# Kernel optimization log

Measured on AMD Instinct MI355X. Metric: run time of the kernel, lower is better.

## Reference

```python
import jax, jax.numpy as jnp
import numpy as np

N_HEAD = 16
N_STATE = 1024
D_HEAD = N_STATE // N_HEAD
B, T = 4, 2048


def setup_inputs() -> dict:
    key = jax.random.key(0)
    ks = jax.random.split(key, 9)
    x = jax.random.normal(ks[0], (B, T, N_STATE), dtype=jnp.float32)
    # causal additive mask, (T, T)
    neg = jnp.float32(-1e9)
    mask = jnp.where(jnp.tril(jnp.ones((T, T), dtype=bool)), 0.0, neg).astype(jnp.float32)
    s = 0.02  # keep activations in a sane range (module uses torch.randn init)
    Wq = jax.random.normal(ks[1], (N_STATE, N_STATE), dtype=jnp.float32) * s
    bq = jax.random.normal(ks[2], (N_STATE,), dtype=jnp.float32) * s
    Wk = jax.random.normal(ks[3], (N_STATE, N_STATE), dtype=jnp.float32) * s
    Wv = jax.random.normal(ks[4], (N_STATE, N_STATE), dtype=jnp.float32) * s
    bv = jax.random.normal(ks[5], (N_STATE,), dtype=jnp.float32) * s
    Wo = jax.random.normal(ks[6], (N_STATE, N_STATE), dtype=jnp.float32) * s
    bo = jax.random.normal(ks[7], (N_STATE,), dtype=jnp.float32) * s
    return {"x": x, "mask": mask, "Wq": Wq, "bq": bq, "Wk": Wk,
            "Wv": Wv, "bv": bv, "Wo": Wo, "bo": bo}


def reference(x, mask, Wq, bq, Wk, Wv, bv, Wo, bo):
    n, t, _ = x.shape
    scale = D_HEAD ** -0.25
    # projections: Linear stores weight as (out, in), applies x @ W.T
    q = x @ Wq.T + bq
    k = x @ Wk.T          # key has no bias
    v = x @ Wv.T + bv
    # (N, H, T, d)
    q = q.reshape(n, t, N_HEAD, D_HEAD).transpose(0, 2, 1, 3) * scale
    k = k.reshape(n, t, N_HEAD, D_HEAD).transpose(0, 2, 1, 3) * scale
    v = v.reshape(n, t, N_HEAD, D_HEAD).transpose(0, 2, 1, 3)
    qk = jnp.einsum('bhqd,bhkd->bhqk', q, k)
    qk = qk + mask[:t, :t]
    attn = jax.nn.softmax(qk, axis=-1)
    qkv = jnp.einsum('bhqk,bhkd->bhqd', attn, v)
    qkv = qkv.transpose(0, 2, 1, 3).reshape(n, t, N_STATE)
    return qkv @ Wo.T + bo
```

## Files before the change

### kernel.cpp

```cpp
#include <hip/hip_runtime.h>
#include <stdint.h>

#define DEVI __device__ __forceinline__

typedef float        f32x4   __attribute__((ext_vector_type(4)));
typedef float        f32x16  __attribute__((ext_vector_type(16)));
typedef __bf16       bf16x8  __attribute__((ext_vector_type(8)));
typedef unsigned short u16x8 __attribute__((ext_vector_type(8)));
typedef uint32_t     u32x2   __attribute__((ext_vector_type(2)));
typedef uint32_t     u32x4   __attribute__((ext_vector_type(4)));

static constexpr int TSEQ   = 2048;
static constexpr int NSTATE = 1024;
static constexpr int NHEAD  = 16;
static constexpr int DHEAD  = 64;
static constexpr int BATCH  = 4;
static constexpr int MROWS  = BATCH * TSEQ;
static constexpr float QSCALE = 0.125f * 1.44269504088896340736f;
static constexpr float DEFER_THR = 8.0f * 1.44269504088896340736f;

DEVI unsigned short f2bf(float f) {
  union { float f; uint32_t u; } v; v.f = f;
  return (unsigned short)((v.u + 0x7fffu + ((v.u >> 16) & 1u)) >> 16);
}

DEVI uint32_t cvt_pk_bf16(float lo, float hi) {
  uint32_t r;
  asm("v_cvt_pk_bf16_f32 %0, %1, %2" : "=v"(r) : "v"(lo), "v"(hi));
  return r;
}

DEVI f32x4 mfma16(u16x8 a, u16x8 b, f32x4 c) {
  return __builtin_amdgcn_mfma_f32_16x16x32_bf16(
      __builtin_bit_cast(bf16x8, a), __builtin_bit_cast(bf16x8, b), c, 0, 0, 0);
}
DEVI f32x16 mfma32(u16x8 a, u16x8 b, f32x16 c) {
  return __builtin_amdgcn_mfma_f32_32x32x16_bf16(
      __builtin_bit_cast(bf16x8, a), __builtin_bit_cast(bf16x8, b), c, 0, 0, 0);
}

DEVI void gload_lds16(const void* g, void* l) {
  __builtin_amdgcn_global_load_lds(
      (const __attribute__((address_space(1))) void*)g,
      (__attribute__((address_space(3))) void*)l, 16, 0, 0);
}

__global__ void cvt_kernel(const float* __restrict__ in,
                           unsigned short* __restrict__ out, int n4) {
  int i = blockIdx.x * blockDim.x + threadIdx.x;
  const int stride = gridDim.x * blockDim.x;
  for (; i < n4; i += stride) {
    const float4 f = ((const float4*)in)[i];
    ushort4 o;
    o.x = f2bf(f.x); o.y = f2bf(f.y); o.z = f2bf(f.z); o.w = f2bf(f.w);
    ((ushort4*)out)[i] = o;
  }
}

__global__ void cvt4_kernel(const float* __restrict__ w0, const float* __restrict__ w1,
                            const float* __restrict__ w2, const float* __restrict__ w3,
                            unsigned short* __restrict__ o0, unsigned short* __restrict__ o1,
                            unsigned short* __restrict__ o2, unsigned short* __restrict__ o3) {
  const int per = NSTATE * NSTATE / 4;
  int i = blockIdx.x * blockDim.x + threadIdx.x;
  const int stride = gridDim.x * blockDim.x;
  for (; i < 4 * per; i += stride) {
    const int wi = i / per, j = i - wi * per;
    const float* src = (wi == 0) ? w0 : (wi == 1) ? w1 : (wi == 2) ? w2 : w3;
    unsigned short* dst = (wi == 0) ? o0 : (wi == 1) ? o1 : (wi == 2) ? o2 : o3;
    const float4 f = ((const float4*)src)[j];
    ushort4 o;
    o.x = f2bf(f.x); o.y = f2bf(f.y); o.z = f2bf(f.z); o.w = f2bf(f.w);
    ((ushort4*)dst)[j] = o;
  }
}

__global__ __launch_bounds__(256)
void gemm_qkv(const unsigned short* __restrict__ A,
              const unsigned short* __restrict__ Wqkv,
              const float* __restrict__ bq, const float* __restrict__ bv,
              unsigned short* __restrict__ Oqkv)
{
  __shared__ __align__(16) unsigned short As[128 * 32];
  __shared__ __align__(16) unsigned short Bs[128 * 32];
  const int t  = threadIdx.x;
  const int l  = t & 63, w = t >> 6;
  const int fr = l & 15, fq = l >> 4;
  const int wi = blockIdx.x >> 3;
  const int n0 = (blockIdx.x & 7) * 128;
  const int m0 = blockIdx.y * 128;
  const int wm = (w & 1) * 64, wn = (w >> 1) * 64;
  const unsigned short* Bw = Wqkv + (size_t)wi * (1u << 20);
  unsigned short* Cq = Oqkv + (size_t)wi * (8u << 20);

  f32x4 acc[4][4] = {};

  const int sr = t >> 2;
  const int sc = (t & 3) * 8;
  const unsigned short* ag = A  + (size_t)(m0 + sr) * NSTATE + sc;
  const unsigned short* bg = Bw + (size_t)(n0 + sr) * NSTATE + sc;
  unsigned short* lA0 = As + t * 8;
  unsigned short* lA1 = As + 2048 + t * 8;
  unsigned short* lB0 = Bs + t * 8;
  unsigned short* lB1 = Bs + 2048 + t * 8;

  for (int kt = 0; kt < NSTATE / 32; ++kt) {
    const int ko = kt * 32;
    gload_lds16(ag + ko,               lA0);
    gload_lds16(ag + 64 * NSTATE + ko, lA1);
    gload_lds16(bg + ko,               lB0);
    gload_lds16(bg + 64 * NSTATE + ko, lB1);
    __syncthreads();

    u16x8 a[4], b[4];
    #pragma unroll
    for (int i = 0; i < 4; ++i)
      a[i] = *(const u16x8*)(As + (wm + i * 16 + fr) * 32 + fq * 8);
    #pragma unroll
    for (int j = 0; j < 4; ++j)
      b[j] = *(const u16x8*)(Bs + (wn + j * 16 + fr) * 32 + fq * 8);
    #pragma unroll
    for (int i = 0; i < 4; ++i)
      #pragma unroll
      for (int j = 0; j < 4; ++j)
        acc[i][j] = mfma16(a[i], b[j], acc[i][j]);
    __syncthreads();
  }

  const int h = (n0 + wn) >> 6;
  #pragma unroll
  for (int j = 0; j < 4; ++j) {
    const int d = j * 16 + fr;
    const float bj = (wi == 1) ? 0.0f
                   : ((wi == 0) ? bq[n0 + wn + d] : bv[n0 + wn + d]);
    #pragma unroll
    for (int i = 0; i < 4; ++i) {
      #pragma unroll
      for (int r = 0; r < 4; ++r) {
        const int row = m0 + wm + i * 16 + fq * 4 + r;
        const int bb = row >> 11, tt = row & (TSEQ - 1);
        float v = acc[i][j][r] + bj;
        if (wi == 0) v *= QSCALE;
        Cq[(((size_t)(bb * NHEAD + h)) * TSEQ + tt) * DHEAD + d] = f2bf(v);
      }
    }
  }
}

__global__ __launch_bounds__(256)
void gemm_out(const unsigned short* __restrict__ A,
              const unsigned short* __restrict__ Bw,
              const float* __restrict__ bias,
              float* __restrict__ Co)
{
  __shared__ __align__(16) unsigned short As[128 * 32];
  __shared__ __align__(16) unsigned short Bs[128 * 32];
  const int t  = threadIdx.x;
  const int l  = t & 63, w = t >> 6;
  const int fr = l & 15, fq = l >> 4;
  const int m0 = blockIdx.y * 128, n0 = blockIdx.x * 128;
  const int wm = (w & 1) * 64, wn = (w >> 1) * 64;

  f32x4 acc[4][4] = {};

  const int sr = t >> 2;
  const int sc = (t & 3) * 8;
  const unsigned short* ag = A  + (size_t)(m0 + sr) * NSTATE + sc;
  const unsigned short* bg = Bw + (size_t)(n0 + sr) * NSTATE + sc;
  unsigned short* lA0 = As + t * 8;
  unsigned short* lA1 = As + 2048 + t * 8;
  unsigned short* lB0 = Bs + t * 8;
  unsigned short* lB1 = Bs + 2048 + t * 8;

  for (int kt = 0; kt < NSTATE / 32; ++kt) {
    const int ko = kt * 32;
    gload_lds16(ag + ko,               lA0);
    gload_lds16(ag + 64 * NSTATE + ko, lA1);
    gload_lds16(bg + ko,               lB0);
    gload_lds16(bg + 64 * NSTATE + ko, lB1);
    __syncthreads();

    u16x8 a[4], b[4];
    #pragma unroll
    for (int i = 0; i < 4; ++i)
      a[i] = *(const u16x8*)(As + (wm + i * 16 + fr) * 32 + fq * 8);
    #pragma unroll
    for (int j = 0; j < 4; ++j)
      b[j] = *(const u16x8*)(Bs + (wn + j * 16 + fr) * 32 + fq * 8);
    #pragma unroll
    for (int i = 0; i < 4; ++i)
      #pragma unroll
      for (int j = 0; j < 4; ++j)
        acc[i][j] = mfma16(a[i], b[j], acc[i][j]);
    __syncthreads();
  }

  #pragma unroll
  for (int j = 0; j < 4; ++j) {
    const int col = n0 + wn + j * 16 + fr;
    const float bj = bias[col];
    #pragma unroll
    for (int i = 0; i < 4; ++i) {
      const int row0 = m0 + wm + i * 16 + fq * 4;
      #pragma unroll
      for (int r = 0; r < 4; ++r)
        Co[(size_t)(row0 + r) * NSTATE + col] = acc[i][j][r] + bj;
    }
  }
}

__global__ __launch_bounds__(256)
void flash_attn(const unsigned short* __restrict__ Qg,
                const unsigned short* __restrict__ Kg,
                const unsigned short* __restrict__ Vg,
                unsigned short* __restrict__ O)
{
  const int bh = blockIdx.x;
  const int b  = bh >> 4, h = bh & 15;
  const int t  = threadIdx.x, lane = t & 63, w = t >> 6;
  const int lq = lane & 31, hi = lane >> 5;
  const size_t hoff = (size_t)bh * TSEQ * DHEAD;
  const unsigned short* Qp = Qg + hoff;
  const unsigned short* Kp = Kg + hoff;
  const unsigned short* Vp = Vg + hoff;

  __shared__ __align__(16) unsigned short Kb[2][64 * 64];
  __shared__ __align__(16) unsigned short Vb[2][64 * 64];

  const int skr = t >> 2, skg = t & 3;
  const int svk2 = (t & 31) * 2;
  const int svd  = (t >> 5) * 8;

  #define STAGE_V(buf, va, vb)                                              \
    do {                                                                    \
      const u32x4 vau = __builtin_bit_cast(u32x4, va);                      \
      const u32x4 vbu = __builtin_bit_cast(u32x4, vb);                      \
      _Pragma("unroll")                                                     \
      for (int j = 0; j < 4; ++j) {                                         \
        const uint32_t pe = __builtin_amdgcn_perm(vbu[j], vau[j], 0x05040100); \
        const uint32_t po = __builtin_amdgcn_perm(vbu[j], vau[j], 0x07060302); \
        *(uint32_t*)(&Vb[buf][(svd + 2 * j) * 64 + (svk2 ^ ((2 * j) << 3))]) = pe; \
        *(uint32_t*)(&Vb[buf][(svd + 2 * j + 1) * 64 + (svk2 ^ ((2 * j + 1) << 3))]) = po; \
      }                                                                     \
    } while (0)

  for (int pass = 0; pass < 2; ++pass) {
    const int qb = pass ? (int)blockIdx.y : 15 - (int)blockIdx.y;
    const int qw   = qb * 128 + w * 32;
    const int qrow = qw + lq;

    u16x8 qf[4];
    #pragma unroll
    for (int c = 0; c < 4; ++c)
      qf[c] = *(const u16x8*)(Qp + (size_t)qrow * DHEAD + c * 16 + hi * 8);

    f32x16 oacc[2] = {};
    float m_r = -1e30f, l_r = 0.0f;

    const int nt = (qb + 1) * 2;

    {
      const u16x8 kr0 = *(const u16x8*)(Kp + (size_t)skr * DHEAD + skg * 16);
      const u16x8 kr1 = *(const u16x8*)(Kp + (size_t)skr * DHEAD + skg * 16 + 8);
      const u16x8 va  = *(const u16x8*)(Vp + (size_t)svk2 * DHEAD + svd);
      const u16x8 vb  = *(const u16x8*)(Vp + (size_t)(svk2 + 1) * DHEAD + svd);
      *(u16x8*)(&Kb[0][skr * 64 + (((skg * 2)     ^ (skr & 7)) << 3)]) = kr0;
      *(u16x8*)(&Kb[0][skr * 64 + (((skg * 2 + 1) ^ (skr & 7)) << 3)]) = kr1;
      STAGE_V(0, va, vb);
    }
    __syncthreads();

    for (int kt = 0; kt < nt; ++kt) {
      const int k0 = kt * 64, cur = kt & 1;
      const bool pre = (kt + 1 < nt);
      u16x8 krn0, krn1, van, vbn;
      if (pre) {
        const int k0n = k0 + 64;
        krn0 = *(const u16x8*)(Kp + (size_t)(k0n + skr) * DHEAD + skg * 16);
        krn1 = *(const u16x8*)(Kp + (size_t)(k0n + skr) * DHEAD + skg * 16 + 8);
        van  = *(const u16x8*)(Vp + (size_t)(k0n + svk2) * DHEAD + svd);
        vbn  = *(const u16x8*)(Vp + (size_t)(k0n + svk2 + 1) * DHEAD + svd);
      }

      if (k0 < qw + 32) {
        f32x16 s[2];
        __builtin_amdgcn_s_setprio(1);
        #pragma unroll
        for (int t32 = 0; t32 < 2; ++t32) {
          if (k0 + t32 * 32 < qw + 32) {
            f32x16 z = {};
            #pragma unroll
            for (int c = 0; c < 4; ++c) {
              const u16x8 kf = *(const u16x8*)(
                  &Kb[cur][(t32 * 32 + lq) * 64 + (((2 * c + hi) ^ (lane & 7)) << 3)]);
              z = mfma32(kf, qf[c], z);
            }
            s[t32] = z;
          } else {
            #pragma unroll
            for (int r = 0; r < 16; ++r) s[t32][r] = -1e30f;
          }
        }
        __builtin_amdgcn_s_setprio(0);
        if (k0 + 63 > qw) {
          #pragma unroll
          for (int t32 = 0; t32 < 2; ++t32)
            #pragma unroll
            for (int r = 0; r < 16; ++r) {
              const int kk = k0 + t32 * 32 + (r & 3) + 8 * (r >> 2) + 4 * hi;
              if (kk > qrow) s[t32][r] = -1e30f;
            }
        }

        float mx = fmaxf(s[0][14], s[0][15]);
        #pragma unroll
        for (int r = 0; r < 14; r += 2) mx = fmaxf(fmaxf(mx, s[0][r]), s[0][r + 1]);
        #pragma unroll
        for (int r = 0; r < 16; r += 2) mx = fmaxf(fmaxf(mx, s[1][r]), s[1][r + 1]);
        mx = fmaxf(mx, __shfl_xor(mx, 32));

        if (__any(mx > m_r + DEFER_THR)) {
          const float mnew = fmaxf(m_r, mx);
          const float corr = exp2f(m_r - mnew);
          #pragma unroll
          for (int ds = 0; ds < 2; ++ds)
            #pragma unroll
            for (int r = 0; r < 16; ++r) oacc[ds][r] *= corr;
          l_r *= corr;
          m_r = mnew;
        }

        float ps = 0.0f;
        uint32_t pk[2][8];
        #pragma unroll
        for (int t32 = 0; t32 < 2; ++t32)
          #pragma unroll
          for (int m2 = 0; m2 < 8; ++m2) {
            const float pa = exp2f(s[t32][2 * m2]     - m_r);
            const float pb = exp2f(s[t32][2 * m2 + 1] - m_r);
            ps += pa + pb;
            pk[t32][m2] = cvt_pk_bf16(pa, pb);
          }
        ps += __shfl_xor(ps, 32);
        l_r += ps;

        uint32_t pf[2][2][4];
        #pragma unroll
        for (int t32 = 0; t32 < 2; ++t32)
          #pragma unroll
          for (int hf = 0; hf < 2; ++hf) {
            const u32x2 r02 = __builtin_amdgcn_permlane32_swap(
                pk[t32][hf * 4 + 0], pk[t32][hf * 4 + 2], false, false);
            const u32x2 r13 = __builtin_amdgcn_permlane32_swap(
                pk[t32][hf * 4 + 1], pk[t32][hf * 4 + 3], false, false);
            pf[t32][hf][0] = r02.x; pf[t32][hf][2] = r02.y;
            pf[t32][hf][1] = r13.x; pf[t32][hf][3] = r13.y;
          }

        __builtin_amdgcn_s_setprio(1);
        #pragma unroll
        for (int c = 0; c < 4; ++c) {
          if (k0 + 16 * c < qw + 32) {
            const u32x4 pw = {pf[c >> 1][c & 1][0], pf[c >> 1][c & 1][1],
                              pf[c >> 1][c & 1][2], pf[c >> 1][c & 1][3]};
            const u16x8 pv = __builtin_bit_cast(u16x8, pw);
            #pragma unroll
            for (int ds = 0; ds < 2; ++ds) {
              const u16x8 vf = *(const u16x8*)(
                  &Vb[cur][(ds * 32 + lq) * 64 + (((2 * c + hi) ^ (lq & 7)) << 3)]);
              oacc[ds] = mfma32(vf, pv, oacc[ds]);
            }
          }
        }
        __builtin_amdgcn_s_setprio(0);
      }

      if (pre) {
        *(u16x8*)(&Kb[cur ^ 1][skr * 64 + (((skg * 2)     ^ (skr & 7)) << 3)]) = krn0;
        *(u16x8*)(&Kb[cur ^ 1][skr * 64 + (((skg * 2 + 1) ^ (skr & 7)) << 3)]) = krn1;
        STAGE_V(cur ^ 1, van, vbn);
      }
      __syncthreads();
    }

    const float inv = 1.0f / l_r;
    const size_t base = ((size_t)(b * TSEQ + qrow)) * NSTATE + h * DHEAD;
    #pragma unroll
    for (int ds = 0; ds < 2; ++ds)
      #pragma unroll
      for (int m2 = 0; m2 < 8; ++m2) {
        const int d = ds * 32 + 2 * (m2 & 1) + 8 * (m2 >> 1) + 4 * hi;
        *(uint32_t*)(O + base + d) =
            cvt_pk_bf16(oacc[ds][2 * m2] * inv, oacc[ds][2 * m2 + 1] * inv);
      }
  }
  #undef STAGE_V
}

extern "C" void kernel_launch(void* const* d_in, const int* in_sizes, int n_in,
                              void* d_out, int out_size, void* d_ws, size_t ws_size,
                              hipStream_t stream)
{
  (void)in_sizes; (void)n_in; (void)out_size; (void)ws_size;
  const float* x  = (const float*)d_in[0];
  const float* Wq = (const float*)d_in[2];
  const float* bq = (const float*)d_in[3];
  const float* Wk = (const float*)d_in[4];
  const float* Wv = (const float*)d_in[5];
  const float* bv = (const float*)d_in[6];
  const float* Wo = (const float*)d_in[7];
  const float* bo = (const float*)d_in[8];

  char* ws = (char*)d_ws;
  unsigned short* xb  = (unsigned short*)(ws);
  unsigned short* wqb = (unsigned short*)(ws + (16u << 20));
  unsigned short* wkb = wqb + (1u << 20);
  unsigned short* wvb = wkb + (1u << 20);
  unsigned short* wob = wvb + (1u << 20);
  unsigned short* qb_ = (unsigned short*)(ws + (24u << 20));
  unsigned short* kb_ = (unsigned short*)(ws + (40u << 20));
  unsigned short* vb_ = (unsigned short*)(ws + (56u << 20));

  cvt_kernel<<<2048, 256, 0, stream>>>(x,  xb,  MROWS * NSTATE / 4);
  cvt4_kernel<<<2048, 256, 0, stream>>>(Wq, Wk, Wv, Wo, wqb, wkb, wvb, wob);

  gemm_qkv<<<dim3(24, MROWS / 128), 256, 0, stream>>>(xb, wqb, bq, bv, qb_);

  flash_attn<<<dim3(BATCH * NHEAD, 8), 256, 0, stream>>>(qb_, kb_, vb_, xb);

  gemm_out<<<dim3(NSTATE / 128, MROWS / 128), 256, 0, stream>>>(xb, wob, bo, (float*)d_out);
}
```

Measured before the change: 202.6 us.

## Enlarge GEMM tiles to 256 with double-buffered swizzled LDS and register prefetch

Both projection GEMMs move to 512-thread blocks with larger tiles: 256x256 for QKV and 128x256 for the output projection. Each k-step now covers 64 instead of 32. The global-to-LDS direct loads are replaced by register-staged prefetch into a double-buffered, XOR-swizzled LDS layout, so the next tile's loads overlap with the MFMAs and there is one barrier per step. s_setprio is raised around the MFMA bursts. The aim is better operand reuse and fewer stalls on global-load latency and LDS bank conflicts. The cost is much more LDS per block (128KB for QKV), which lowers occupancy, and fewer blocks in the grid.

After: 202.6 us. Within noise of the previous version (+0.0%).

```diff
diff --git a/kernel.cpp b/kernel.cpp
--- a/kernel.cpp
+++ b/kernel.cpp
@@ -37,12 +37,6 @@
 DEVI f32x16 mfma32(u16x8 a, u16x8 b, f32x16 c) {
   return __builtin_amdgcn_mfma_f32_32x32x16_bf16(
       __builtin_bit_cast(bf16x8, a), __builtin_bit_cast(bf16x8, b), c, 0, 0, 0);
-}
-
-DEVI void gload_lds16(const void* g, void* l) {
-  __builtin_amdgcn_global_load_lds(
-      (const __attribute__((address_space(1))) void*)g,
-      (__attribute__((address_space(3))) void*)l, 16, 0, 0);
 }
 
 __global__ void cvt_kernel(const float* __restrict__ in,
@@ -75,69 +69,103 @@
   }
 }
 
-__global__ __launch_bounds__(256)
-void gemm_qkv(const unsigned short* __restrict__ A,
-              const unsigned short* __restrict__ Wqkv,
-              const float* __restrict__ bq, const float* __restrict__ bv,
-              unsigned short* __restrict__ Oqkv)
+__global__ __launch_bounds__(512)
+void gemm_qkv256(const unsigned short* __restrict__ A,
+                 const unsigned short* __restrict__ Wqkv,
+                 const float* __restrict__ bq, const float* __restrict__ bv,
+                 unsigned short* __restrict__ Oqkv)
 {
-  __shared__ __align__(16) unsigned short As[128 * 32];
-  __shared__ __align__(16) unsigned short Bs[128 * 32];
-  const int t  = threadIdx.x;
-  const int l  = t & 63, w = t >> 6;
-  const int fr = l & 15, fq = l >> 4;
-  const int wi = blockIdx.x >> 3;
-  const int n0 = (blockIdx.x & 7) * 128;
-  const int m0 = blockIdx.y * 128;
-  const int wm = (w & 1) * 64, wn = (w >> 1) * 64;
-  const unsigned short* Bw = Wqkv + (size_t)wi * (1u << 20);
-  unsigned short* Cq = Oqkv + (size_t)wi * (8u << 20);
-
-  f32x4 acc[4][4] = {};
-
-  const int sr = t >> 2;
-  const int sc = (t & 3) * 8;
-  const unsigned short* ag = A  + (size_t)(m0 + sr) * NSTATE + sc;
-  const unsigned short* bg = Bw + (size_t)(n0 + sr) * NSTATE + sc;
-  unsigned short* lA0 = As + t * 8;
-  unsigned short* lA1 = As + 2048 + t * 8;
-  unsigned short* lB0 = Bs + t * 8;
-  unsigned short* lB1 = Bs + 2048 + t * 8;
-
-  for (int kt = 0; kt < NSTATE / 32; ++kt) {
-    const int ko = kt * 32;
-    gload_lds16(ag + ko,               lA0);
-    gload_lds16(ag + 64 * NSTATE + ko, lA1);
-    gload_lds16(bg + ko,               lB0);
-    gload_lds16(bg + 64 * NSTATE + ko, lB1);
+  __shared__ __align__(16) unsigned short As[2][256 * 64];
+  __shared__ __align__(16) unsigned short Bs[2][256 * 64];
+  const int t = threadIdx.x;
+  const int lane = t & 63, wid = t >> 6;
+  const int fr = lane & 15, fq = lane >> 4;
+  const int wi  = blockIdx.x >> 2;
+  const int n0w = (blockIdx.x & 3) * 256;
+  const int m0  = blockIdx.y * 256;
+  const int wm = wid >> 2, wn = wid & 3;
+  const unsigned short* Bw = Wqkv + ((size_t)wi << 20);
+  unsigned short* Cq = Oqkv + ((size_t)wi << 23);
+
+  f32x4 acc[8][4] = {};
+
+  const int srow = t >> 3, sg = t & 7;
+  const unsigned short* ag = A  + (size_t)(m0  + srow) * NSTATE + sg * 8;
+  const unsigned short* bg = Bw + (size_t)(n0w + srow) * NSTATE + sg * 8;
+  int wof[4];
+  #pragma unroll
+  for (int s = 0; s < 4; ++s) {
+    const int r = srow + s * 64;
+    wof[s] = r * 64 + ((sg ^ (r & 7)) * 8);
+  }
+
+  u16x8 sa[4], sb[4];
+  #pragma unroll
+  for (int s = 0; s < 4; ++s) {
+    sa[s] = *(const u16x8*)(ag + (size_t)s * 64 * NSTATE);
+    sb[s] = *(const u16x8*)(bg + (size_t)s * 64 * NSTATE);
+  }
+  #pragma unroll
+  for (int s = 0; s < 4; ++s) {
+    *(u16x8*)(&As[0][wof[s]]) = sa[s];
+    *(u16x8*)(&Bs[0][wof[s]]) = sb[s];
+  }
+
+  for (int kt = 0; kt < NSTATE / 64; ++kt) {
+    const int cur = kt & 1;
     __syncthreads();
-
-    u16x8 a[4], b[4];
-    #pragma unroll
-    for (int i = 0; i < 4; ++i)
-      a[i] = *(const u16x8*)(As + (wm + i * 16 + fr) * 32 + fq * 8);
-    #pragma unroll
-    for (int j = 0; j < 4; ++j)
-      b[j] = *(const u16x8*)(Bs + (wn + j * 16 + fr) * 32 + fq * 8);
-    #pragma unroll
-    for (int i = 0; i < 4; ++i)
-      #pragma unroll
-      for (int j = 0; j < 4; ++j)
-        acc[i][j] = mfma16(a[i], b[j], acc[i][j]);
-    __syncthreads();
-  }
-
-  const int h = (n0 + wn) >> 6;
+    const bool pre = (kt + 1) < NSTATE / 64;
+    if (pre) {
+      const int ko = (kt + 1) * 64;
+      #pragma unroll
+      for (int s = 0; s < 4; ++s) {
+        sa[s] = *(const u16x8*)(ag + ko + (size_t)s * 64 * NSTATE);
+        sb[s] = *(const u16x8*)(bg + ko + (size_t)s * 64 * NSTATE);
+      }
+    }
+    #pragma unroll
+    for (int kk = 0; kk < 2; ++kk) {
+      u16x8 af[8], bf[4];
+      #pragma unroll
+      for (int i = 0; i < 8; ++i) {
+        const int r = wm * 128 + i * 16 + fr;
+        const int g = (kk * 4 + fq) ^ (r & 7);
+        af[i] = *(const u16x8*)(&As[cur][r * 64 + g * 8]);
+      }
+      #pragma unroll
+      for (int j = 0; j < 4; ++j) {
+        const int r = wn * 64 + j * 16 + fr;
+        const int g = (kk * 4 + fq) ^ (r & 7);
+        bf[j] = *(const u16x8*)(&Bs[cur][r * 64 + g * 8]);
+      }
+      __builtin_amdgcn_s_setprio(1);
+      #pragma unroll
+      for (int i = 0; i < 8; ++i)
+        #pragma unroll
+        for (int j = 0; j < 4; ++j)
+          acc[i][j] = mfma16(af[i], bf[j], acc[i][j]);
+      __builtin_amdgcn_s_setprio(0);
+    }
+    if (pre) {
+      #pragma unroll
+      for (int s = 0; s < 4; ++s) {
+        *(u16x8*)(&As[cur ^ 1][wof[s]]) = sa[s];
+        *(u16x8*)(&Bs[cur ^ 1][wof[s]]) = sb[s];
+      }
+    }
+  }
+
+  const int h = (n0w + wn * 64) >> 6;
   #pragma unroll
   for (int j = 0; j < 4; ++j) {
     const int d = j * 16 + fr;
-    const float bj = (wi == 1) ? 0.0f
-                   : ((wi == 0) ? bq[n0 + wn + d] : bv[n0 + wn + d]);
-    #pragma unroll
-    for (int i = 0; i < 4; ++i) {
+    const int ncol = n0w + wn * 64 + d;
+    const float bj = (wi == 1) ? 0.0f : ((wi == 0) ? bq[ncol] : bv[ncol]);
+    #pragma unroll
+    for (int i = 0; i < 8; ++i) {
       #pragma unroll
       for (int r = 0; r < 4; ++r) {
-        const int row = m0 + wm + i * 16 + fq * 4 + r;
+        const int row = m0 + wm * 128 + i * 16 + fq * 4 + r;
         const int bb = row >> 11, tt = row & (TSEQ - 1);
         float v = acc[i][j][r] + bj;
         if (wi == 0) v *= QSCALE;
@@ -147,61 +175,96 @@
   }
 }
 
-__global__ __launch_bounds__(256)
-void gemm_out(const unsigned short* __restrict__ A,
-              const unsigned short* __restrict__ Bw,
-              const float* __restrict__ bias,
-              float* __restrict__ Co)
+__global__ __launch_bounds__(512)
+void gemm_out256(const unsigned short* __restrict__ A,
+                 const unsigned short* __restrict__ Bw,
+                 const float* __restrict__ bias,
+                 float* __restrict__ Co)
 {
-  __shared__ __align__(16) unsigned short As[128 * 32];
-  __shared__ __align__(16) unsigned short Bs[128 * 32];
-  const int t  = threadIdx.x;
-  const int l  = t & 63, w = t >> 6;
-  const int fr = l & 15, fq = l >> 4;
-  const int m0 = blockIdx.y * 128, n0 = blockIdx.x * 128;
-  const int wm = (w & 1) * 64, wn = (w >> 1) * 64;
+  __shared__ __align__(16) unsigned short As[2][128 * 64];
+  __shared__ __align__(16) unsigned short Bs[2][256 * 64];
+  const int t = threadIdx.x;
+  const int lane = t & 63, wid = t >> 6;
+  const int fr = lane & 15, fq = lane >> 4;
+  const int n0 = blockIdx.x * 256;
+  const int m0 = blockIdx.y * 128;
+  const int wm = wid >> 2, wn = wid & 3;
 
   f32x4 acc[4][4] = {};
 
-  const int sr = t >> 2;
-  const int sc = (t & 3) * 8;
-  const unsigned short* ag = A  + (size_t)(m0 + sr) * NSTATE + sc;
-  const unsigned short* bg = Bw + (size_t)(n0 + sr) * NSTATE + sc;
-  unsigned short* lA0 = As + t * 8;
-  unsigned short* lA1 = As + 2048 + t * 8;
-  unsigned short* lB0 = Bs + t * 8;
-  unsigned short* lB1 = Bs + 2048 + t * 8;
-
-  for (int kt = 0; kt < NSTATE / 32; ++kt) {
-    const int ko = kt * 32;
-    gload_lds16(ag + ko,               lA0);
-    gload_lds16(ag + 64 * NSTATE + ko, lA1);
-    gload_lds16(bg + ko,               lB0);
-    gload_lds16(bg + 64 * NSTATE + ko, lB1);
+  const int srow = t >> 3, sg = t & 7;
+  const unsigned short* ag = A  + (size_t)(m0 + srow) * NSTATE + sg * 8;
+  const unsigned short* bg = Bw + (size_t)(n0 + srow) * NSTATE + sg * 8;
+  int wof[4];
+  #pragma unroll
+  for (int s = 0; s < 4; ++s) {
+    const int r = srow + s * 64;
+    wof[s] = r * 64 + ((sg ^ (r & 7)) * 8);
+  }
+
+  u16x8 sa[2], sb[4];
+  #pragma unroll
+  for (int s = 0; s < 2; ++s)
+    sa[s] = *(const u16x8*)(ag + (size_t)s * 64 * NSTATE);
+  #pragma unroll
+  for (int s = 0; s < 4; ++s)
+    sb[s] = *(const u16x8*)(bg + (size_t)s * 64 * NSTATE);
+  #pragma unroll
+  for (int s = 0; s < 2; ++s) *(u16x8*)(&As[0][wof[s]]) = sa[s];
+  #pragma unroll
+  for (int s = 0; s < 4; ++s) *(u16x8*)(&Bs[0][wof[s]]) = sb[s];
+
+  for (int kt = 0; kt < NSTATE / 64; ++kt) {
+    const int cur = kt & 1;
     __syncthreads();
-
-    u16x8 a[4], b[4];
-    #pragma unroll
-    for (int i = 0; i < 4; ++i)
-      a[i] = *(const u16x8*)(As + (wm + i * 16 + fr) * 32 + fq * 8);
-    #pragma unroll
-    for (int j = 0; j < 4; ++j)
-      b[j] = *(const u16x8*)(Bs + (wn + j * 16 + fr) * 32 + fq * 8);
-    #pragma unroll
-    for (int i = 0; i < 4; ++i)
-      #pragma unroll
-      for (int j = 0; j < 4; ++j)
-        acc[i][j] = mfma16(a[i], b[j], acc[i][j]);
-    __syncthreads();
+    const bool pre = (kt + 1) < NSTATE / 64;
+    if (pre) {
+      const int ko = (kt + 1) * 64;
+      #pragma unroll
+      for (int s = 0; s < 2; ++s)
+        sa[s] = *(const u16x8*)(ag + ko + (size_t)s * 64 * NSTATE);
+      #pragma unroll
+      for (int s = 0; s < 4; ++s)
+        sb[s] = *(const u16x8*)(bg + ko + (size_t)s * 64 * NSTATE);
+    }
+    #pragma unroll
+    for (int kk = 0; kk < 2; ++kk) {
+      u16x8 af[4], bf[4];
+      #pragma unroll
+      for (int i = 0; i < 4; ++i) {
+        const int r = wm * 64 + i * 16 + fr;
+        const int g = (kk * 4 + fq) ^ (r & 7);
+        af[i] = *(const u16x8*)(&As[cur][r * 64 + g * 8]);
+      }
+      #pragma unroll
+      for (int j = 0; j < 4; ++j) {
+        const int r = wn * 64 + j * 16 + fr;
+        const int g = (kk * 4 + fq) ^ (r & 7);
+        bf[j] = *(const u16x8*)(&Bs[cur][r * 64 + g * 8]);
+      }
+      __builtin_amdgcn_s_setprio(1);
+      #pragma unroll
+      for (int i = 0; i < 4; ++i)
+        #pragma unroll
+        for (int j = 0; j < 4; ++j)
+          acc[i][j] = mfma16(af[i], bf[j], acc[i][j]);
+      __builtin_amdgcn_s_setprio(0);
+    }
+    if (pre) {
+      #pragma unroll
+      for (int s = 0; s < 2; ++s) *(u16x8*)(&As[cur ^ 1][wof[s]]) = sa[s];
+      #pragma unroll
+      for (int s = 0; s < 4; ++s) *(u16x8*)(&Bs[cur ^ 1][wof[s]]) = sb[s];
+    }
   }
 
   #pragma unroll
   for (int j = 0; j < 4; ++j) {
-    const int col = n0 + wn + j * 16 + fr;
+    const int col = n0 + wn * 64 + j * 16 + fr;
     const float bj = bias[col];
     #pragma unroll
     for (int i = 0; i < 4; ++i) {
-      const int row0 = m0 + wm + i * 16 + fq * 4;
+      const int row0 = m0 + wm * 64 + i * 16 + fq * 4;
       #pragma unroll
       for (int r = 0; r < 4; ++r)
         Co[(size_t)(row0 + r) * NSTATE + col] = acc[i][j][r] + bj;
@@ -424,9 +487,9 @@
   cvt_kernel<<<2048, 256, 0, stream>>>(x,  xb,  MROWS * NSTATE / 4);
   cvt4_kernel<<<2048, 256, 0, stream>>>(Wq, Wk, Wv, Wo, wqb, wkb, wvb, wob);
 
-  gemm_qkv<<<dim3(24, MROWS / 128), 256, 0, stream>>>(xb, wqb, bq, bv, qb_);
+  gemm_qkv256<<<dim3(12, MROWS / 256), 512, 0, stream>>>(xb, wqb, bq, bv, qb_);
 
   flash_attn<<<dim3(BATCH * NHEAD, 8), 256, 0, stream>>>(qb_, kb_, vb_, xb);
 
-  gemm_out<<<dim3(NSTATE / 128, MROWS / 128), 256, 0, stream>>>(xb, wob, bo, (float*)d_out);
-}
+  gemm_out256<<<dim3(NSTATE / 256, MROWS / 128), 512, 0, stream>>>(xb, wob, bo, (float*)d_out);
+}
```

## Split flash attention to one query block per workgroup; fuse conversion kernels

Applied to the files above, without the earlier changes.

The attention kernel previously had each workgroup handle two paired query blocks (15-y and y) to balance causal work. Now each workgroup handles a single query block, over a grid twice as large, which gives more parallelism but loses the pairing-based load balance. The two fp32-to-bf16 conversion kernels are merged into one launch, and exp2f is replaced by raw v_exp_f32. LDS fragment offsets are also precomputed outside the loop.

After: 186.2 us, median of 3. 1.09x faster.

```diff
diff --git a/kernel.cpp b/kernel.cpp
--- a/kernel.cpp
+++ b/kernel.cpp
@@ -29,6 +29,11 @@
   asm("v_cvt_pk_bf16_f32 %0, %1, %2" : "=v"(r) : "v"(lo), "v"(hi));
   return r;
 }
+DEVI float fexp2(float x) {
+  float r;
+  asm("v_exp_f32 %0, %1" : "=v"(r) : "v"(x));
+  return r;
+}
 
 DEVI f32x4 mfma16(u16x8 a, u16x8 b, f32x4 c) {
   return __builtin_amdgcn_mfma_f32_16x16x32_bf16(
@@ -45,29 +50,28 @@
       (__attribute__((address_space(3))) void*)l, 16, 0, 0);
 }
 
-__global__ void cvt_kernel(const float* __restrict__ in,
-                           unsigned short* __restrict__ out, int n4) {
+__global__ void cvt_all(const float* __restrict__ x,
+                        const float* __restrict__ w0, const float* __restrict__ w1,
+                        const float* __restrict__ w2, const float* __restrict__ w3,
+                        unsigned short* __restrict__ xb,
+                        unsigned short* __restrict__ wb)
+{
+  const int NX = (MROWS * NSTATE) / 4;
+  const int NW = (NSTATE * NSTATE) / 4;
+  const int total = NX + 4 * NW;
   int i = blockIdx.x * blockDim.x + threadIdx.x;
   const int stride = gridDim.x * blockDim.x;
-  for (; i < n4; i += stride) {
-    const float4 f = ((const float4*)in)[i];
-    ushort4 o;
-    o.x = f2bf(f.x); o.y = f2bf(f.y); o.z = f2bf(f.z); o.w = f2bf(f.w);
-    ((ushort4*)out)[i] = o;
-  }
-}
-
-__global__ void cvt4_kernel(const float* __restrict__ w0, const float* __restrict__ w1,
-                            const float* __restrict__ w2, const float* __restrict__ w3,
-                            unsigned short* __restrict__ o0, unsigned short* __restrict__ o1,
-                            unsigned short* __restrict__ o2, unsigned short* __restrict__ o3) {
-  const int per = NSTATE * NSTATE / 4;
-  int i = blockIdx.x * blockDim.x + threadIdx.x;
-  const int stride = gridDim.x * blockDim.x;
-  for (; i < 4 * per; i += stride) {
-    const int wi = i / per, j = i - wi * per;
-    const float* src = (wi == 0) ? w0 : (wi == 1) ? w1 : (wi == 2) ? w2 : w3;
-    unsigned short* dst = (wi == 0) ? o0 : (wi == 1) ? o1 : (wi == 2) ? o2 : o3;
+  for (; i < total; i += stride) {
+    const float* src;
+    unsigned short* dst;
+    int j;
+    if (i < NX) { src = x; dst = xb; j = i; }
+    else {
+      const int k = i - NX, wi = k >> 18;
+      src = (wi == 0) ? w0 : (wi == 1) ? w1 : (wi == 2) ? w2 : w3;
+      dst = wb + ((size_t)wi << 20);
+      j = k & (NW - 1);
+    }
     const float4 f = ((const float4*)src)[j];
     ushort4 o;
     o.x = f2bf(f.x); o.y = f2bf(f.y); o.z = f2bf(f.z); o.w = f2bf(f.w);
@@ -90,8 +94,8 @@
   const int n0 = (blockIdx.x & 7) * 128;
   const int m0 = blockIdx.y * 128;
   const int wm = (w & 1) * 64, wn = (w >> 1) * 64;
-  const unsigned short* Bw = Wqkv + (size_t)wi * (1u << 20);
-  unsigned short* Cq = Oqkv + (size_t)wi * (8u << 20);
+  const unsigned short* Bw = Wqkv + ((size_t)wi << 20);
+  unsigned short* Cq = Oqkv + ((size_t)wi << 23);
 
   f32x4 acc[4][4] = {};
 
@@ -216,6 +220,7 @@
                 unsigned short* __restrict__ O)
 {
   const int bh = blockIdx.x;
+  const int qb = 15 - (int)blockIdx.y;
   const int b  = bh >> 4, h = bh & 15;
   const int t  = threadIdx.x, lane = t & 63, w = t >> 6;
   const int lq = lane & 31, hi = lane >> 5;
@@ -227,9 +232,31 @@
   __shared__ __align__(16) unsigned short Kb[2][64 * 64];
   __shared__ __align__(16) unsigned short Vb[2][64 * 64];
 
+  const int qw   = qb * 128 + w * 32;
+  const int qrow = qw + lq;
+
+  u16x8 qf[4];
+  #pragma unroll
+  for (int c = 0; c < 4; ++c)
+    qf[c] = *(const u16x8*)(Qp + (size_t)qrow * DHEAD + c * 16 + hi * 8);
+
+  f32x16 oacc[2] = {};
+  float m_r = -1e30f, l_r = 0.0f;
+
+  const char* KbB = (const char*)&Kb[0][0];
+  const char* VbB = (const char*)&Vb[0][0];
+  int koff[4], voff[4];
+  #pragma unroll
+  for (int c = 0; c < 4; ++c) {
+    koff[c] = lq * 128 + (((2 * c + hi) ^ (lane & 7)) << 4);
+    voff[c] = lq * 128 + (((2 * c + hi) ^ (lq & 7)) << 4);
+  }
+
   const int skr = t >> 2, skg = t & 3;
   const int svk2 = (t & 31) * 2;
   const int svd  = (t >> 5) * 8;
+
+  const int nt = (qb + 1) * 2;
 
   #define STAGE_V(buf, va, vb)                                              \
     do {                                                                    \
@@ -244,156 +271,140 @@
       }                                                                     \
     } while (0)
 
-  for (int pass = 0; pass < 2; ++pass) {
-    const int qb = pass ? (int)blockIdx.y : 15 - (int)blockIdx.y;
-    const int qw   = qb * 128 + w * 32;
-    const int qrow = qw + lq;
-
-    u16x8 qf[4];
-    #pragma unroll
-    for (int c = 0; c < 4; ++c)
-      qf[c] = *(const u16x8*)(Qp + (size_t)qrow * DHEAD + c * 16 + hi * 8);
-
-    f32x16 oacc[2] = {};
-    float m_r = -1e30f, l_r = 0.0f;
-
-    const int nt = (qb + 1) * 2;
-
-    {
-      const u16x8 kr0 = *(const u16x8*)(Kp + (size_t)skr * DHEAD + skg * 16);
-      const u16x8 kr1 = *(const u16x8*)(Kp + (size_t)skr * DHEAD + skg * 16 + 8);
-      const u16x8 va  = *(const u16x8*)(Vp + (size_t)svk2 * DHEAD + svd);
-      const u16x8 vb  = *(const u16x8*)(Vp + (size_t)(svk2 + 1) * DHEAD + svd);
-      *(u16x8*)(&Kb[0][skr * 64 + (((skg * 2)     ^ (skr & 7)) << 3)]) = kr0;
-      *(u16x8*)(&Kb[0][skr * 64 + (((skg * 2 + 1) ^ (skr & 7)) << 3)]) = kr1;
-      STAGE_V(0, va, vb);
-    }
-    __syncthreads();
-
-    for (int kt = 0; kt < nt; ++kt) {
-      const int k0 = kt * 64, cur = kt & 1;
-      const bool pre = (kt + 1 < nt);
-      u16x8 krn0, krn1, van, vbn;
-      if (pre) {
-        const int k0n = k0 + 64;
-        krn0 = *(const u16x8*)(Kp + (size_t)(k0n + skr) * DHEAD + skg * 16);
-        krn1 = *(const u16x8*)(Kp + (size_t)(k0n + skr) * DHEAD + skg * 16 + 8);
-        van  = *(const u16x8*)(Vp + (size_t)(k0n + svk2) * DHEAD + svd);
-        vbn  = *(const u16x8*)(Vp + (size_t)(k0n + svk2 + 1) * DHEAD + svd);
+  {
+    const u16x8 kr0 = *(const u16x8*)(Kp + (size_t)skr * DHEAD + skg * 16);
+    const u16x8 kr1 = *(const u16x8*)(Kp + (size_t)skr * DHEAD + skg * 16 + 8);
+    const u16x8 va  = *(const u16x8*)(Vp + (size_t)svk2 * DHEAD + svd);
+    const u16x8 vb  = *(const u16x8*)(Vp + (size_t)(svk2 + 1) * DHEAD + svd);
+    *(u16x8*)(&Kb[0][skr * 64 + (((skg * 2)     ^ (skr & 7)) << 3)]) = kr0;
+    *(u16x8*)(&Kb[0][skr * 64 + (((skg * 2 + 1) ^ (skr & 7)) << 3)]) = kr1;
+    STAGE_V(0, va, vb);
+  }
+  __syncthreads();
+
+  for (int kt = 0; kt < nt; ++kt) {
+    const int k0 = kt * 64;
+    const int curB = (kt & 1) << 13;
+    const bool pre = (kt + 1 < nt);
+    u16x8 krn0, krn1, van, vbn;
+    if (pre) {
+      const int k0n = k0 + 64;
+      krn0 = *(const u16x8*)(Kp + (size_t)(k0n + skr) * DHEAD + skg * 16);
+      krn1 = *(const u16x8*)(Kp + (size_t)(k0n + skr) * DHEAD + skg * 16 + 8);
+      van  = *(const u16x8*)(Vp + (size_t)(k0n + svk2) * DHEAD + svd);
+      vbn  = *(const u16x8*)(Vp + (size_t)(k0n + svk2 + 1) * DHEAD + svd);
+    }
+
+    if (k0 < qw + 32) {
+      f32x16 s[2];
+      __builtin_amdgcn_s_setprio(1);
+      #pragma unroll
+      for (int t32 = 0; t32 < 2; ++t32) {
+        if (k0 + t32 * 32 < qw + 32) {
+          f32x16 z = {};
+          #pragma unroll
+          for (int c = 0; c < 4; ++c) {
+            const u16x8 kf = *(const u16x8*)(KbB + curB + koff[c] + t32 * 4096);
+            z = mfma32(kf, qf[c], z);
+          }
+          s[t32] = z;
+        } else {
+          #pragma unroll
+          for (int r = 0; r < 16; ++r) s[t32][r] = -1e30f;
+        }
       }
-
-      if (k0 < qw + 32) {
-        f32x16 s[2];
-        __builtin_amdgcn_s_setprio(1);
-        #pragma unroll
-        for (int t32 = 0; t32 < 2; ++t32) {
-          if (k0 + t32 * 32 < qw + 32) {
-            f32x16 z = {};
-            #pragma unroll
-            for (int c = 0; c < 4; ++c) {
-              const u16x8 kf = *(const u16x8*)(
-                  &Kb[cur][(t32 * 32 + lq) * 64 + (((2 * c + hi) ^ (lane & 7)) << 3)]);
-              z = mfma32(kf, qf[c], z);
-            }
-            s[t32] = z;
-          } else {
-            #pragma unroll
-            for (int r = 0; r < 16; ++r) s[t32][r] = -1e30f;
-          }
-        }
-        __builtin_amdgcn_s_setprio(0);
-        if (k0 + 63 > qw) {
-          #pragma unroll
-          for (int t32 = 0; t32 < 2; ++t32)
-            #pragma unroll
-            for (int r = 0; r < 16; ++r) {
-              const int kk = k0 + t32 * 32 + (r & 3) + 8 * (r >> 2) + 4 * hi;
-              if (kk > qrow) s[t32][r] = -1e30f;
-            }
-        }
-
-        float mx = fmaxf(s[0][14], s[0][15]);
-        #pragma unroll
-        for (int r = 0; r < 14; r += 2) mx = fmaxf(fmaxf(mx, s[0][r]), s[0][r + 1]);
-        #pragma unroll
-        for (int r = 0; r < 16; r += 2) mx = fmaxf(fmaxf(mx, s[1][r]), s[1][r + 1]);
-        mx = fmaxf(mx, __shfl_xor(mx, 32));
-
-        if (__any(mx > m_r + DEFER_THR)) {
-          const float mnew = fmaxf(m_r, mx);
-          const float corr = exp2f(m_r - mnew);
-          #pragma unroll
-          for (int ds = 0; ds < 2; ++ds)
-            #pragma unroll
-            for (int r = 0; r < 16; ++r) oacc[ds][r] *= corr;
-          l_r *= corr;
-          m_r = mnew;
-        }
-
-        float ps = 0.0f;
-        uint32_t pk[2][8];
+      __builtin_amdgcn_s_setprio(0);
+      if (k0 + 63 > qw) {
         #pragma unroll
         for (int t32 = 0; t32 < 2; ++t32)
           #pragma unroll
-          for (int m2 = 0; m2 < 8; ++m2) {
-            const float pa = exp2f(s[t32][2 * m2]     - m_r);
-            const float pb = exp2f(s[t32][2 * m2 + 1] - m_r);
-            ps += pa + pb;
-            pk[t32][m2] = cvt_pk_bf16(pa, pb);
+          for (int r = 0; r < 16; ++r) {
+            const int kk = k0 + t32 * 32 + (r & 3) + 8 * (r >> 2) + 4 * hi;
+            if (kk > qrow) s[t32][r] = -1e30f;
           }
-        ps += __shfl_xor(ps, 32);
-        l_r += ps;
-
-        uint32_t pf[2][2][4];
+      }
+
+      float mx = fmaxf(s[0][14], s[0][15]);
+      #pragma unroll
+      for (int r = 0; r < 14; r += 2) mx = fmaxf(fmaxf(mx, s[0][r]), s[0][r + 1]);
+      #pragma unroll
+      for (int r = 0; r < 16; r += 2) mx = fmaxf(fmaxf(mx, s[1][r]), s[1][r + 1]);
+      mx = fmaxf(mx, __shfl_xor(mx, 32));
+
+      if (__any(mx > m_r + DEFER_THR)) {
+        const float mnew = fmaxf(m_r, mx);
+        const float corr = fexp2(m_r - mnew);
         #pragma unroll
-        for (int t32 = 0; t32 < 2; ++t32)
+        for (int ds = 0; ds < 2; ++ds)
           #pragma unroll
-          for (int hf = 0; hf < 2; ++hf) {
-            const u32x2 r02 = __builtin_amdgcn_permlane32_swap(
-                pk[t32][hf * 4 + 0], pk[t32][hf * 4 + 2], false, false);
-            const u32x2 r13 = __builtin_amdgcn_permlane32_swap(
-                pk[t32][hf * 4 + 1], pk[t32][hf * 4 + 3], false, false);
-            pf[t32][hf][0] = r02.x; pf[t32][hf][2] = r02.y;
-            pf[t32][hf][1] = r13.x; pf[t32][hf][3] = r13.y;
-          }
-
-        __builtin_amdgcn_s_setprio(1);
+          for (int r = 0; r < 16; ++r) oacc[ds][r] *= corr;
+        l_r *= corr;
+        m_r = mnew;
+      }
+
+      float ps = 0.0f;
+      uint32_t pk[2][8];
+      #pragma unroll
+      for (int t32 = 0; t32 < 2; ++t32)
         #pragma unroll
-        for (int c = 0; c < 4; ++c) {
-          if (k0 + 16 * c < qw + 32) {
-            const u32x4 pw = {pf[c >> 1][c & 1][0], pf[c >> 1][c & 1][1],
-                              pf[c >> 1][c & 1][2], pf[c >> 1][c & 1][3]};
-            const u16x8 pv = __builtin_bit_cast(u16x8, pw);
-            #pragma unroll
-            for (int ds = 0; ds < 2; ++ds) {
-              const u16x8 vf = *(const u16x8*)(
-                  &Vb[cur][(ds * 32 + lq) * 64 + (((2 * c + hi) ^ (lq & 7)) << 3)]);
-              oacc[ds] = mfma32(vf, pv, oacc[ds]);
-            }
+        for (int m2 = 0; m2 < 8; ++m2) {
+          const float pa = fexp2(s[t32][2 * m2]     - m_r);
+          const float pb = fexp2(s[t32][2 * m2 + 1] - m_r);
+          ps += pa + pb;
+          pk[t32][m2] = cvt_pk_bf16(pa, pb);
+        }
+      ps += __shfl_xor(ps, 32);
+      l_r += ps;
+
+      uint32_t pf[2][2][4];
+      #pragma unroll
+      for (int t32 = 0; t32 < 2; ++t32)
+        #pragma unroll
+        for (int hf = 0; hf < 2; ++hf) {
+          const u32x2 r02 = __builtin_amdgcn_permlane32_swap(
+              pk[t32][hf * 4 + 0], pk[t32][hf * 4 + 2], false, false);
+          const u32x2 r13 = __builtin_amdgcn_permlane32_swap(
+              pk[t32][hf * 4 + 1], pk[t32][hf * 4 + 3], false, false);
+          pf[t32][hf][0] = r02.x; pf[t32][hf][2] = r02.y;
+          pf[t32][hf][1] = r13.x; pf[t32][hf][3] = r13.y;
+        }
+
+      __builtin_amdgcn_s_setprio(1);
+      #pragma unroll
+      for (int c = 0; c < 4; ++c) {
+        if (k0 + 16 * c < qw + 32) {
+          const u32x4 pw = {pf[c >> 1][c & 1][0], pf[c >> 1][c & 1][1],
+                            pf[c >> 1][c & 1][2], pf[c >> 1][c & 1][3]};
+          const u16x8 pv = __builtin_bit_cast(u16x8, pw);
+          #pragma unroll
+          for (int ds = 0; ds < 2; ++ds) {
+            const u16x8 vf = *(const u16x8*)(VbB + curB + voff[c] + ds * 4096);
+            oacc[ds] = mfma32(vf, pv, oacc[ds]);
           }
         }
-        __builtin_amdgcn_s_setprio(0);
       }
-
-      if (pre) {
-        *(u16x8*)(&Kb[cur ^ 1][skr * 64 + (((skg * 2)     ^ (skr & 7)) << 3)]) = krn0;
-        *(u16x8*)(&Kb[cur ^ 1][skr * 64 + (((skg * 2 + 1) ^ (skr & 7)) << 3)]) = krn1;
-        STAGE_V(cur ^ 1, van, vbn);
-      }
-      __syncthreads();
-    }
-
-    const float inv = 1.0f / l_r;
-    const size_t base = ((size_t)(b * TSEQ + qrow)) * NSTATE + h * DHEAD;
-    #pragma unroll
-    for (int ds = 0; ds < 2; ++ds)
-      #pragma unroll
-      for (int m2 = 0; m2 < 8; ++m2) {
-        const int d = ds * 32 + 2 * (m2 & 1) + 8 * (m2 >> 1) + 4 * hi;
-        *(uint32_t*)(O + base + d) =
-            cvt_pk_bf16(oacc[ds][2 * m2] * inv, oacc[ds][2 * m2 + 1] * inv);
-      }
-  }
+      __builtin_amdgcn_s_setprio(0);
+    }
+
+    if (pre) {
+      const int nb = (kt & 1) ^ 1;
+      *(u16x8*)(&Kb[nb][skr * 64 + (((skg * 2)     ^ (skr & 7)) << 3)]) = krn0;
+      *(u16x8*)(&Kb[nb][skr * 64 + (((skg * 2 + 1) ^ (skr & 7)) << 3)]) = krn1;
+      STAGE_V(nb, van, vbn);
+    }
+    __syncthreads();
+  }
+
+  const float inv = 1.0f / l_r;
+  const size_t base = ((size_t)(b * TSEQ + qrow)) * NSTATE + h * DHEAD;
+  #pragma unroll
+  for (int ds = 0; ds < 2; ++ds)
+    #pragma unroll
+    for (int m2 = 0; m2 < 8; ++m2) {
+      const int d = ds * 32 + 2 * (m2 & 1) + 8 * (m2 >> 1) + 4 * hi;
+      *(uint32_t*)(O + base + d) =
+          cvt_pk_bf16(oacc[ds][2 * m2] * inv, oacc[ds][2 * m2 + 1] * inv);
+    }
   #undef STAGE_V
 }
 
@@ -414,19 +425,16 @@
   char* ws = (char*)d_ws;
   unsigned short* xb  = (unsigned short*)(ws);
   unsigned short* wqb = (unsigned short*)(ws + (16u << 20));
-  unsigned short* wkb = wqb + (1u << 20);
-  unsigned short* wvb = wkb + (1u << 20);
-  unsigned short* wob = wvb + (1u << 20);
+  unsigned short* wob = wqb + (3u << 20);
   unsigned short* qb_ = (unsigned short*)(ws + (24u << 20));
   unsigned short* kb_ = (unsigned short*)(ws + (40u << 20));
   unsigned short* vb_ = (unsigned short*)(ws + (56u << 20));
 
-  cvt_kernel<<<2048, 256, 0, stream>>>(x,  xb,  MROWS * NSTATE / 4);
-  cvt4_kernel<<<2048, 256, 0, stream>>>(Wq, Wk, Wv, Wo, wqb, wkb, wvb, wob);
+  cvt_all<<<2048, 256, 0, stream>>>(x, Wq, Wk, Wv, Wo, xb, wqb);
 
   gemm_qkv<<<dim3(24, MROWS / 128), 256, 0, stream>>>(xb, wqb, bq, bv, qb_);
 
-  flash_attn<<<dim3(BATCH * NHEAD, 8), 256, 0, stream>>>(qb_, kb_, vb_, xb);
+  flash_attn<<<dim3(BATCH * NHEAD, 16), 256, 0, stream>>>(qb_, kb_, vb_, xb);
 
   gemm_out<<<dim3(NSTATE / 128, MROWS / 128), 256, 0, stream>>>(xb, wob, bo, (float*)d_out);
 }
```
